# Optimization experiments

Hardware: AMD Instinct MI355X
Metric: run time of the kernel (lower is better)

## Reference

```python
import jax, jax.numpy as jnp
import numpy as np

LW = (1.0, 1.0, 1.0)          # loss_weight
TLW = (0.1, 1.0)              # Total_loss_weight
TRIPLET_W = np.array([1.17236407, 1.0166286, 1.19620973, 0.5544405, 0.63531401, 0.51258428,
                      1.08866652, 1.15795989, 1.07389395, 0.98728399, 1.12754142, 1.05953744,
                      1.16945323, 1.15512349, 1.02097204, 1.15795989, 1.07147279, 0.50627649,
                      1.07147279, 0.61697221, 1.16367678, 1.0231585, 1.18416106, 1.04329092,
                      1.10645159, 1.18416106, 1.15795989, 1.16367678, 0.73949534, 0.78760821,
                      1.08617476, 1.00805777], dtype=np.float32)


def _lsa(cost):
    """Hungarian algorithm (Jonker-Volgenant / e-maxx potentials), equivalent to
    scipy.optimize.linear_sum_assignment for rectangular matrices."""
    cost = np.asarray(cost, dtype=np.float64)
    T = cost.shape[0] > cost.shape[1]
    C = cost.T if T else cost
    n, m = C.shape
    u = np.zeros(n + 1); v = np.zeros(m + 1)
    p = np.zeros(m + 1, dtype=np.int64)
    way = np.zeros(m + 1, dtype=np.int64)
    for i in range(1, n + 1):
        p[0] = i; j0 = 0
        minv = np.full(m + 1, np.inf)
        used = np.zeros(m + 1, dtype=bool)
        while True:
            used[j0] = True
            i0 = p[j0]
            cur = C[i0 - 1] - u[i0] - v[1:]
            free = ~used[1:]
            upd = free & (cur < minv[1:])
            minv[1:] = np.where(upd, cur, minv[1:])
            way[1:] = np.where(upd, j0, way[1:])
            js = np.where(free)[0]
            j1 = js[np.argmin(minv[1:][js])] + 1
            delta = minv[j1]
            u[p[used]] += delta
            v[used] -= delta
            minv[~used] -= delta
            j0 = j1
            if p[j0] == 0:
                break
        while j0:
            j1 = way[j0]; p[j0] = p[j1]; j0 = j1
    cols = np.arange(m)
    sel = p[1:] > 0
    r, c = p[1:][sel] - 1, cols[sel]
    order = np.argsort(r)
    r, c = r[order], c[order]
    return (c, r) if T else (r, c)


def _cost_matrix(pred_head, pred_rel, pred_tail, iid, vid, tid):
    # per-element weighted CrossEntropyLoss over a single sample reduces to plain
    # -log_softmax at the target (the class weight cancels in the 'mean' reduction)
    def nll(logits, tgt, C):
        logp = jax.nn.log_softmax(logits, axis=-1)           # [B,Q,C]
        oh = jax.nn.one_hot(tgt, C, dtype=logp.dtype)        # [B,G,C]
        return -jnp.einsum('bqc,bgc->bqg', logp, oh)         # [B,Q,G]
    return (LW[0] * nll(pred_head, iid, 9)
            + LW[1] * nll(pred_rel, vid, 13)
            + LW[2] * nll(pred_tail, tid, 2))


def setup_inputs() -> dict:
    key = jax.random.key(0)
    ks = jax.random.split(key, 12)
    B, Q, G = 256, 300, 16
    return {
        'pred_head': jax.random.normal(ks[0], (B, Q, 9), jnp.float32),
        'pred_rel': jax.random.normal(ks[1], (B, Q, 13), jnp.float32),
        'pred_tail': jax.random.normal(ks[2], (B, Q, 2), jnp.float32),
        'IVT': jax.random.normal(ks[3], (B, 32), jnp.float32),
        'instrumentId': jax.random.randint(ks[4], (B, G), 0, 9, jnp.int32),
        'verbId': jax.random.randint(ks[5], (B, G), 0, 13, jnp.int32),
        'targetId': jax.random.randint(ks[6], (B, G), 0, 2, jnp.int32),
        'instrument': jax.random.randint(ks[7], (B, G), 0, 9, jnp.int32),
        'verb': jax.random.randint(ks[8], (B, G), 0, 13, jnp.int32),
        'target': jax.random.randint(ks[9], (B, G), 0, 2, jnp.int32),
        'triplet': jax.random.randint(ks[10], (B, 32), 0, 2, jnp.int32),
        'mask': jnp.ones((B, G), jnp.int32),
    }


def reference(pred_head, pred_rel, pred_tail, IVT, instrumentId, verbId, targetId,
              instrument, verb, target, triplet, mask):
    sim = _cost_matrix(pred_head, pred_rel, pred_tail, instrumentId, verbId, targetId)  # [B,Q,G]
    # masked_fill(inf) on invalid gt columns (no-op for all-ones mask, kept for fidelity)
    sim_filled = jnp.where((mask == 0)[:, None, :], jnp.inf, sim)
    sim_np = np.asarray(jax.device_get(sim_filled))
    mask_np = np.asarray(jax.device_get(mask))
    b_list, r_list, c_list = [], [], []
    for i in range(sim_np.shape[0]):
        nval = int(mask_np[i].sum())
        r, c = _lsa(sim_np[i][:, :nval])
        b_list.append(np.full(len(r), i, dtype=np.int64))
        r_list.append(r); c_list.append(c)
    b_idx = jnp.asarray(np.concatenate(b_list))
    r_idx = jnp.asarray(np.concatenate(r_list))
    c_idx = jnp.asarray(np.concatenate(c_list))
    loss1 = sim_filled[b_idx, r_idx, c_idx].mean()
    # weighted BCEWithLogitsLoss (weight scales per-element loss; mean over all elements)
    x = IVT
    t = triplet.astype(jnp.float32)
    bce = jnp.maximum(x, 0.0) - x * t + jnp.log1p(jnp.exp(-jnp.abs(x)))
    loss5 = (jnp.asarray(TRIPLET_W) * bce).mean()
    return TLW[0] * loss1 + TLW[1] * loss5
```

## Files before the change

### kernel.cpp

```cpp
#include <hip/hip_runtime.h>
#include <hip/hip_bf16.h>


#define NQ 300
#define NG 16
#define NT 5
#define SCR_STR 25

__device__ const float d_tw[32] = {
    1.17236407f, 1.0166286f,  1.19620973f, 0.5544405f,  0.63531401f, 0.51258428f,
    1.08866652f, 1.15795989f, 1.07389395f, 0.98728399f, 1.12754142f, 1.05953744f,
    1.16945323f, 1.15512349f, 1.02097204f, 1.15795989f, 1.07147279f, 0.50627649f,
    1.07147279f, 0.61697221f, 1.16367678f, 1.0231585f,  1.18416106f, 1.04329092f,
    1.10645159f, 1.18416106f, 1.15795989f, 1.16367678f, 0.73949534f, 0.78760821f,
    1.08617476f, 1.00805777f};

__device__ __forceinline__ float wave_min_bcast(float x) {
    int t;
    t = __builtin_amdgcn_update_dpp(__float_as_int(x), __float_as_int(x), 0x111, 0xF, 0xF, false);
    x = fminf(x, __int_as_float(t));
    t = __builtin_amdgcn_update_dpp(__float_as_int(x), __float_as_int(x), 0x112, 0xF, 0xF, false);
    x = fminf(x, __int_as_float(t));
    t = __builtin_amdgcn_update_dpp(__float_as_int(x), __float_as_int(x), 0x114, 0xF, 0xF, false);
    x = fminf(x, __int_as_float(t));
    t = __builtin_amdgcn_update_dpp(__float_as_int(x), __float_as_int(x), 0x118, 0xF, 0xF, false);
    x = fminf(x, __int_as_float(t));
    t = __builtin_amdgcn_update_dpp(__float_as_int(x), __float_as_int(x), 0x142, 0xF, 0xF, false);
    x = fminf(x, __int_as_float(t));
    t = __builtin_amdgcn_update_dpp(__float_as_int(x), __float_as_int(x), 0x143, 0xF, 0xF, false);
    x = fminf(x, __int_as_float(t));
    return __int_as_float(__builtin_amdgcn_readlane(__float_as_int(x), 63));
}

__global__ __launch_bounds__(64) void SetCriterion_14482629722575_kernel(
    const float* __restrict__ ph, const float* __restrict__ pr,
    const float* __restrict__ pt, const float* __restrict__ ivt,
    const int* __restrict__ iid, const int* __restrict__ vid,
    const int* __restrict__ tid, const int* __restrict__ trip,
    float* __restrict__ out)
{
    const int b    = blockIdx.x;
    const int lane = threadIdx.x;
    const float FINF = 3.0e38f;

    __shared__ float cost[NG * NQ];
    __shared__ float scr[64 * SCR_STR];
    __shared__ float uinit[NG + 1];
    __shared__ int   sgi[NG], sgv[NG], sgt[NG];

    if (lane < NG) {
        sgi[lane] = iid[b * NG + lane];
        sgv[lane] = vid[b * NG + lane];
        sgt[lane] = tid[b * NG + lane];
    }
    __syncthreads();

    int gi[NG], gv[NG], gc[NG];
    #pragma unroll
    for (int i = 0; i < NG; i++) { gi[i] = sgi[i]; gv[i] = sgv[i]; gc[i] = sgt[i]; }

    float rmin[NG]; int rjm[NG];
    #pragma unroll
    for (int i = 0; i < NG; i++) { rmin[i] = FINF; rjm[i] = 0; }

    float* myrow = &scr[lane * SCR_STR];
    for (int q = lane; q < NQ; q += 64) {
        {
            const float* x = ph + ((size_t)b * NQ + q) * 9;
            float r[9];
            #pragma unroll
            for (int c = 0; c < 9; c++) r[c] = x[c];
            float m = r[0];
            #pragma unroll
            for (int c = 1; c < 9; c++) m = fmaxf(m, r[c]);
            float sE = 0.f;
            #pragma unroll
            for (int c = 0; c < 9; c++) sE += expf(r[c] - m);
            float lse = m + logf(sE);
            #pragma unroll
            for (int c = 0; c < 9; c++) myrow[c] = lse - r[c];
        }
        {
            const float* x = pr + ((size_t)b * NQ + q) * 13;
            float r[13];
            #pragma unroll
            for (int c = 0; c < 13; c++) r[c] = x[c];
            float m = r[0];
            #pragma unroll
            for (int c = 1; c < 13; c++) m = fmaxf(m, r[c]);
            float sE = 0.f;
            #pragma unroll
            for (int c = 0; c < 13; c++) sE += expf(r[c] - m);
            float lse = m + logf(sE);
            #pragma unroll
            for (int c = 0; c < 13; c++) myrow[9 + c] = lse - r[c];
        }
        {
            const float* x = pt + ((size_t)b * NQ + q) * 2;
            float r0 = x[0], r1 = x[1];
            float m = fmaxf(r0, r1);
            float lse = m + logf(expf(r0 - m) + expf(r1 - m));
            myrow[22] = lse - r0;
            myrow[23] = lse - r1;
        }
        #pragma unroll
        for (int i = 0; i < NG; i++) {
            const float c = myrow[gi[i]] + myrow[9 + gv[i]] + myrow[22 + gc[i]];
            cost[i * NQ + q] = c;
            if (c < rmin[i]) { rmin[i] = c; rjm[i] = q + 1; }
        }
    }
    __syncthreads();

    int jm_[NG];
    #pragma unroll
    for (int i = 0; i < NG; i++) {
        const float m = wave_min_bcast(rmin[i]);
        const unsigned long long msk = __ballot(rmin[i] == m);
        const int l0 = (int)__ffsll(msk) - 1;
        jm_[i] = __builtin_amdgcn_readlane(rjm[i], l0);
        if (lane == 0) uinit[i + 1] = m;
    }
    __syncthreads();

    float v_[NT], minv_[NT];
    int   way_[NT], par_[NT];
    bool  valid[NT];
    #pragma unroll
    for (int t = 0; t < NT; t++) {
        valid[t] = (t * 64 + lane + 1 <= NQ);
        v_[t] = 0.f; par_[t] = 0; way_[t] = 0; minv_[t] = FINF;
    }

    int pending = 0;
    #pragma unroll
    for (int i = 1; i <= NG; i++) {
        const int jm = jm_[i - 1];
        const int slot = (jm - 1) >> 6, owner = (jm - 1) & 63;
        int psel = par_[0];
        #pragma unroll
        for (int t = 1; t < NT; t++) if (slot == t) psel = par_[t];
        const int pcur = __builtin_amdgcn_readlane(psel, owner);
        if (pcur == 0) {
            #pragma unroll
            for (int t = 0; t < NT; t++) if (slot == t && lane == owner) par_[t] = i;
        } else {
            pending |= 1 << (i - 1);
        }
    }

    while (pending) {
        const int r = __ffs(pending);
        pending &= pending - 1;
        #pragma unroll
        for (int t = 0; t < NT; t++) minv_[t] = FINF;
        unsigned usedbits = 0;
        float u0 = uinit[r];
        int i0 = r, j0 = 0, guard = 0;

        while (true) {
            if (j0 && ((j0 - 1) & 63) == lane) usedbits |= 1u << ((j0 - 1) >> 6);

            const int rowbase = (i0 - 1) * NQ;
            float raw[NT];
            #pragma unroll
            for (int t = 0; t < NT; t++) {
                const int j = t * 64 + lane + 1;
                raw[t] = (valid[t] ? cost[rowbase + j - 1] : FINF) - v_[t];
            }

            float lmin = FINF;
            int   lmeta = 0x7FFFFFFF;
            #pragma unroll
            for (int t = 0; t < NT; t++) {
                if (valid[t] && !((usedbits >> t) & 1u)) {
                    const float cur = raw[t] - u0;
                    if (cur < minv_[t]) { minv_[t] = cur; way_[t] = j0; }
                    if (minv_[t] < lmin) {
                        lmin = minv_[t];
                        lmeta = ((t * 64 + lane + 1) << 5) | par_[t];
                    }
                }
            }
            const float delta = wave_min_bcast(lmin);
            const unsigned long long msk = __ballot(lmin == delta);
            const int l0 = (int)__ffsll(msk) - 1;
            const int meta = __builtin_amdgcn_readlane(lmeta, l0);
            const int j1 = meta >> 5, i1 = meta & 31;

            #pragma unroll
            for (int t = 0; t < NT; t++) {
                if ((usedbits >> t) & 1u) v_[t] -= delta;
                else                      minv_[t] -= delta;
            }

            if (i1 == 0) { j0 = j1; break; }

            {
                const int slot = (j1 - 1) >> 6, owner = (j1 - 1) & 63;
                float vsel = v_[0];
                #pragma unroll
                for (int t = 1; t < NT; t++) if (slot == t) vsel = v_[t];
                const float vj1 = __int_as_float(
                    __builtin_amdgcn_readlane(__float_as_int(vsel), owner));
                u0 = cost[(i1 - 1) * NQ + (j1 - 1)] - vj1;
            }
            j0 = j1; i0 = i1;
            if (++guard > 40) break;
        }

        int jj = j0;
        while (jj) {
            const int slot = (jj - 1) >> 6, owner = (jj - 1) & 63;
            int wsel = way_[0];
            #pragma unroll
            for (int t = 1; t < NT; t++) if (slot == t) wsel = way_[t];
            const int wj = __builtin_amdgcn_readlane(wsel, owner);
            int pj;
            if (wj == 0) pj = r;
            else {
                const int s2 = (wj - 1) >> 6, o2 = (wj - 1) & 63;
                int psel = par_[0];
                #pragma unroll
                for (int t = 1; t < NT; t++) if (s2 == t) psel = par_[t];
                pj = __builtin_amdgcn_readlane(psel, o2);
            }
            #pragma unroll
            for (int t = 0; t < NT; t++)
                if (slot == t && ((jj - 1) & 63) == lane) par_[t] = pj;
            jj = wj;
        }
    }

    float s = 0.f;
    #pragma unroll
    for (int t = 0; t < NT; t++) {
        const int j = t * 64 + lane + 1;
        if (valid[t] && par_[t] > 0)
            s += cost[(par_[t] - 1) * NQ + (j - 1)];
    }
    #pragma unroll
    for (int off = 32; off >= 1; off >>= 1) s += __shfl_xor(s, off);

    float bs = 0.f;
    if (lane < 32) {
        const float x  = ivt[b * 32 + lane];
        const float tt = (float)trip[b * 32 + lane];
        bs = d_tw[lane] * (fmaxf(x, 0.f) - x * tt + log1pf(expf(-fabsf(x))));
    }
    #pragma unroll
    for (int off = 32; off >= 1; off >>= 1) bs += __shfl_xor(bs, off);

    if (lane == 0)
        atomicAdd(out, 0.1f * (s / 4096.0f) + bs / 8192.0f);
}

extern "C" void kernel_launch(void* const* d_in, const int* in_sizes, int n_in,
                              void* d_out, int out_size, void* d_ws, size_t ws_size,
                              hipStream_t stream) {
    (void)in_sizes; (void)n_in; (void)d_ws; (void)ws_size; (void)out_size;

    const float* pred_head    = (const float*)d_in[0];
    const float* pred_rel     = (const float*)d_in[1];
    const float* pred_tail    = (const float*)d_in[2];
    const float* IVT          = (const float*)d_in[3];
    const int*   instrumentId = (const int*)d_in[4];
    const int*   verbId       = (const int*)d_in[5];
    const int*   targetId     = (const int*)d_in[6];
    const int*   triplet      = (const int*)d_in[10];

    hipMemsetAsync(d_out, 0, 4, stream);

    SetCriterion_14482629722575_kernel<<<256, 64, 0, stream>>>(
        pred_head, pred_rel, pred_tail, IVT,
        instrumentId, verbId, targetId, triplet, (float*)d_out);
}
```

Baseline: 97.82 us.

## Use four waves per batch for cost build, offload BCE to second wave

The block grows from one wave to four, so the 300-query log-softmax and cost-matrix build is split across 256 threads. Per-wave column minima are merged through shared memory. The BCE term moves to wave 1, and the Hungarian solve stays on wave 0. Initial conflict detection is now computed from register copies of the column argmins, and exp/log use fast intrinsics. This targets the serial prologue, at the cost of more shared memory per block, lower occupancy, and slightly less accurate math.

```diff
diff --git a/kernel.cpp b/kernel.cpp
--- a/kernel.cpp
+++ b/kernel.cpp
@@ -2,6 +2,7 @@
 #include <hip/hip_bf16.h>
 
 
+#define BT 256
 #define NQ 300
 #define NG 16
 #define NT 5
@@ -32,26 +33,29 @@
     return __int_as_float(__builtin_amdgcn_readlane(__float_as_int(x), 63));
 }
 
-__global__ __launch_bounds__(64) void SetCriterion_14482629722575_kernel(
+__global__ __launch_bounds__(BT) void SetCriterion_14482629722575_kernel(
     const float* __restrict__ ph, const float* __restrict__ pr,
     const float* __restrict__ pt, const float* __restrict__ ivt,
     const int* __restrict__ iid, const int* __restrict__ vid,
-    const int* __restrict__ tid, const int* __restrict__ trip,
+    const int* __restrict__ tid_, const int* __restrict__ trip,
     float* __restrict__ out)
 {
     const int b    = blockIdx.x;
-    const int lane = threadIdx.x;
+    const int tid  = threadIdx.x;
+    const int wave = tid >> 6;
+    const int lane = tid & 63;
     const float FINF = 3.0e38f;
 
     __shared__ float cost[NG * NQ];
-    __shared__ float scr[64 * SCR_STR];
-    __shared__ float uinit[NG + 1];
+    __shared__ float scr[BT * SCR_STR];
+    __shared__ float pmin[4][NG];
+    __shared__ int   pjm[4][NG];
     __shared__ int   sgi[NG], sgv[NG], sgt[NG];
 
-    if (lane < NG) {
-        sgi[lane] = iid[b * NG + lane];
-        sgv[lane] = vid[b * NG + lane];
-        sgt[lane] = tid[b * NG + lane];
+    if (tid < NG) {
+        sgi[tid] = iid[b * NG + tid];
+        sgv[tid] = vid[b * NG + tid];
+        sgt[tid] = tid_[b * NG + tid];
     }
     __syncthreads();
 
@@ -63,8 +67,8 @@
     #pragma unroll
     for (int i = 0; i < NG; i++) { rmin[i] = FINF; rjm[i] = 0; }
 
-    float* myrow = &scr[lane * SCR_STR];
-    for (int q = lane; q < NQ; q += 64) {
+    float* myrow = &scr[tid * SCR_STR];
+    for (int q = tid; q < NQ; q += BT) {
         {
             const float* x = ph + ((size_t)b * NQ + q) * 9;
             float r[9];
@@ -75,8 +79,8 @@
             for (int c = 1; c < 9; c++) m = fmaxf(m, r[c]);
             float sE = 0.f;
             #pragma unroll
-            for (int c = 0; c < 9; c++) sE += expf(r[c] - m);
-            float lse = m + logf(sE);
+            for (int c = 0; c < 9; c++) sE += __expf(r[c] - m);
+            const float lse = m + __logf(sE);
             #pragma unroll
             for (int c = 0; c < 9; c++) myrow[c] = lse - r[c];
         }
@@ -90,16 +94,16 @@
             for (int c = 1; c < 13; c++) m = fmaxf(m, r[c]);
             float sE = 0.f;
             #pragma unroll
-            for (int c = 0; c < 13; c++) sE += expf(r[c] - m);
-            float lse = m + logf(sE);
+            for (int c = 0; c < 13; c++) sE += __expf(r[c] - m);
+            const float lse = m + __logf(sE);
             #pragma unroll
             for (int c = 0; c < 13; c++) myrow[9 + c] = lse - r[c];
         }
         {
             const float* x = pt + ((size_t)b * NQ + q) * 2;
-            float r0 = x[0], r1 = x[1];
-            float m = fmaxf(r0, r1);
-            float lse = m + logf(expf(r0 - m) + expf(r1 - m));
+            const float r0 = x[0], r1 = x[1];
+            const float m = fmaxf(r0, r1);
+            const float lse = m + __logf(__expf(r0 - m) + __expf(r1 - m));
             myrow[22] = lse - r0;
             myrow[23] = lse - r1;
         }
@@ -110,18 +114,43 @@
             if (c < rmin[i]) { rmin[i] = c; rjm[i] = q + 1; }
         }
     }
-    __syncthreads();
-
-    int jm_[NG];
+
     #pragma unroll
     for (int i = 0; i < NG; i++) {
         const float m = wave_min_bcast(rmin[i]);
         const unsigned long long msk = __ballot(rmin[i] == m);
         const int l0 = (int)__ffsll(msk) - 1;
-        jm_[i] = __builtin_amdgcn_readlane(rjm[i], l0);
-        if (lane == 0) uinit[i + 1] = m;
+        const int jm = __builtin_amdgcn_readlane(rjm[i], l0);
+        if (lane == 0) { pmin[wave][i] = m; pjm[wave][i] = jm; }
     }
     __syncthreads();
+
+    if (wave == 1) {
+        float bs = 0.f;
+        if (lane < 32) {
+            const float x  = ivt[b * 32 + lane];
+            const float tt = (float)trip[b * 32 + lane];
+            const float e  = __expf(-fabsf(x));
+            bs = d_tw[lane] * (fmaxf(x, 0.f) - x * tt + __logf(1.f + e));
+        }
+        #pragma unroll
+        for (int off = 32; off >= 1; off >>= 1) bs += __shfl_xor(bs, off);
+        if (lane == 0) atomicAdd(out, bs / 8192.0f);
+        return;
+    }
+    if (wave != 0) return;
+
+    float um[NG]; int jm_[NG];
+    #pragma unroll
+    for (int i = 0; i < NG; i++) {
+        float m = pmin[0][i]; int jm = pjm[0][i];
+        #pragma unroll
+        for (int w = 1; w < 4; w++) {
+            const float mw = pmin[w][i]; const int jw = pjm[w][i];
+            if (mw < m) { m = mw; jm = jw; }
+        }
+        um[i] = m; jm_[i] = jm;
+    }
 
     float v_[NT], minv_[NT];
     int   way_[NT], par_[NT];
@@ -134,18 +163,21 @@
 
     int pending = 0;
     #pragma unroll
-    for (int i = 1; i <= NG; i++) {
-        const int jm = jm_[i - 1];
-        const int slot = (jm - 1) >> 6, owner = (jm - 1) & 63;
-        int psel = par_[0];
-        #pragma unroll
-        for (int t = 1; t < NT; t++) if (slot == t) psel = par_[t];
-        const int pcur = __builtin_amdgcn_readlane(psel, owner);
-        if (pcur == 0) {
-            #pragma unroll
-            for (int t = 0; t < NT; t++) if (slot == t && lane == owner) par_[t] = i;
-        } else {
-            pending |= 1 << (i - 1);
+    for (int i = 1; i < NG; i++) {
+        bool conf = false;
+        #pragma unroll
+        for (int k = 0; k < NG; k++)
+            if (k < i && jm_[k] == jm_[i]) conf = true;
+        if (conf) pending |= 1 << i;
+    }
+    #pragma unroll
+    for (int i = 0; i < NG; i++) {
+        if (!((pending >> i) & 1)) {
+            const int jm = jm_[i];
+            const int slot = (jm - 1) >> 6, owner = (jm - 1) & 63;
+            #pragma unroll
+            for (int t = 0; t < NT; t++)
+                if (slot == t && lane == owner) par_[t] = i + 1;
         }
     }
 
@@ -155,7 +187,9 @@
         #pragma unroll
         for (int t = 0; t < NT; t++) minv_[t] = FINF;
         unsigned usedbits = 0;
-        float u0 = uinit[r];
+        float u0 = 0.f;
+        #pragma unroll
+        for (int i = 0; i < NG; i++) if (r == i + 1) u0 = um[i];
         int i0 = r, j0 = 0, guard = 0;
 
         while (true) {
@@ -242,17 +276,8 @@
     #pragma unroll
     for (int off = 32; off >= 1; off >>= 1) s += __shfl_xor(s, off);
 
-    float bs = 0.f;
-    if (lane < 32) {
-        const float x  = ivt[b * 32 + lane];
-        const float tt = (float)trip[b * 32 + lane];
-        bs = d_tw[lane] * (fmaxf(x, 0.f) - x * tt + log1pf(expf(-fabsf(x))));
-    }
-    #pragma unroll
-    for (int off = 32; off >= 1; off >>= 1) bs += __shfl_xor(bs, off);
-
     if (lane == 0)
-        atomicAdd(out, 0.1f * (s / 4096.0f) + bs / 8192.0f);
+        atomicAdd(out, 0.1f * (s / 4096.0f));
 }
 
 extern "C" void kernel_launch(void* const* d_in, const int* in_sizes, int n_in,
@@ -271,7 +296,7 @@
 
     hipMemsetAsync(d_out, 0, 4, stream);
 
-    SetCriterion_14482629722575_kernel<<<256, 64, 0, stream>>>(
+    SetCriterion_14482629722575_kernel<<<256, BT, 0, stream>>>(
         pred_head, pred_rel, pred_tail, IVT,
         instrumentId, verbId, targetId, triplet, (float*)d_out);
 }
```

New measurement: 90.81 us. 1.08x faster.
